# Kernel tuning notes

Hardware: AMD Instinct MI355X
Metric: run time of the kernel (lower is better)

Reference implementation:

```python
import jax, jax.numpy as jnp
import numpy as np

DIM = 1024
KEY = 128
UV = 1024  # dim * mlp_ratio // 2
SCALE = 1.0 / np.sqrt(KEY).astype(np.float32)
NEG_INF = 1e12


def _sinusoidal(n, d):
    # RoPE tables: sin/cos of shape [n, d//2]
    pos = np.arange(n)[:, None].astype(np.float32)
    inv = (1.0 / 10000 ** (np.arange(0, d, 2).astype(np.float32) / d))[None, :]
    ang = pos * inv
    return jnp.asarray(np.sin(ang)), jnp.asarray(np.cos(ang))


def setup_inputs() -> dict:
    key = jax.random.key(0)
    ks = jax.random.split(key, 4)
    B, N = 4, 2048
    hidden_states = jax.random.normal(ks[0], (B, N, DIM), dtype=jnp.float32)
    attention_mask = jax.random.randint(ks[1], (B, N, N), 0, 2).astype(jnp.int32)
    sin, cos = _sinusoidal(N, KEY)
    Wi = jax.random.normal(ks[2], (DIM, UV * 2 + KEY), dtype=jnp.float32) * (DIM ** -0.5)
    bi = jnp.zeros((UV * 2 + KEY,), jnp.float32)
    Wo = jax.random.normal(ks[3], (UV, DIM), dtype=jnp.float32) * (UV ** -0.5)
    bo = jnp.zeros((DIM,), jnp.float32)
    return {
        "hidden_states": hidden_states, "attention_mask": attention_mask,
        "sin": sin, "cos": cos, "Wi": Wi, "bi": bi, "Wo": Wo, "bo": bo,
        "q_gamma": jnp.ones((KEY,), jnp.float32), "q_beta": jnp.zeros((KEY,), jnp.float32),
        "k_gamma": jnp.ones((KEY,), jnp.float32), "k_beta": jnp.zeros((KEY,), jnp.float32),
    }


def _rotary(x, sin, cos):
    # x: [b, n, d]; sin/cos: [n, d//2]; interleaved RoPE, concat layout
    x1, x2 = x[..., 0::2], x[..., 1::2]
    return jnp.concatenate([x1 * cos - x2 * sin, x1 * sin + x2 * cos], axis=-1)


def reference(hidden_states, attention_mask, sin, cos, Wi, bi, Wo, bo,
              q_gamma, q_beta, k_gamma, k_beta):
    x = jax.nn.silu(hidden_states @ Wi + bi)            # [b, n, 2176]
    u, v, qk = x[..., :UV], x[..., UV:2 * UV], x[..., 2 * UV:]
    q = _rotary(qk * q_gamma + q_beta, sin, cos)        # [b, n, 128]
    k = _rotary(qk * k_gamma + k_beta, sin, cos)
    a = jnp.einsum('bmd,bnd->bmn', q, k) * SCALE        # [b, m, n]
    mask = attention_mask != 0
    a = jnp.where(mask, a, -NEG_INF)
    ll = attention_mask.sum(-1, keepdims=True).astype(a.dtype)  # [b, m, 1]
    A = jnp.square(jax.nn.relu(a)) / ll                 # squared_relu normalize
    out = (u * jnp.einsum('bmn,bnd->bmd', A, v)) @ Wo + bo
    return out
```

## Files before the change

kernel.cpp:

```cpp
#include <hip/hip_runtime.h>
#include <hip/hip_bf16.h>
#include <cstdint>

#define DIM   1024
#define KEY   128
#define UV    1024
#define NCOL  (UV*2 + KEY)
#define SEQ   2048
#define BATCH 4
#define MTOT  (BATCH*SEQ)
#define SCALE 0.08838834764831845f

typedef __attribute__((ext_vector_type(8))) short short8;
typedef __attribute__((ext_vector_type(4))) float f32x4;

__device__ inline unsigned short f2b(float x) {
  unsigned int u = __float_as_uint(x);
  unsigned int r = (u + 0x7fffu + ((u >> 16) & 1u)) >> 16;
  return (unsigned short)r;
}
__device__ inline float b2f(unsigned short x) {
  return __uint_as_float(((unsigned int)x) << 16);
}

__device__ inline void gload_lds16(const void* g, void* l) {
  __builtin_amdgcn_global_load_lds(
      (const __attribute__((address_space(1))) unsigned int*)g,
      (__attribute__((address_space(3))) unsigned int*)l, 16, 0, 0);
}

__device__ __forceinline__ void gemm128(
    const unsigned short* __restrict__ A, int lda,
    const unsigned short* __restrict__ Bt, int ldb,
    int K, f32x4 acc[4][4], unsigned short* lds) {
  const int tid  = threadIdx.x;
  const int lane = tid & 63;
  const int wid  = tid >> 6;
  const int wr   = wid >> 1, wc = wid & 1;
  const int fr   = lane & 15;
  const int fq   = lane >> 4;

#pragma unroll
  for (int i = 0; i < 4; ++i)
#pragma unroll
    for (int j = 0; j < 4; ++j) acc[i][j] = (f32x4){0.f, 0.f, 0.f, 0.f};

  auto stage = [&](int k, int d) {
    unsigned short* la = lds + d * 8192;
    unsigned short* lb = la + 4096;
#pragma unroll
    for (int p = 0; p < 2; ++p) {
      int c = p * 256 + tid;
      int r = c >> 2, q = c & 3;
      int qs = q ^ ((r >> 1) & 3);
      gload_lds16(A + (size_t)r * lda + k * 32 + qs * 8,
                  la + (size_t)(p * 256 + wid * 64) * 8);
    }
#pragma unroll
    for (int p = 0; p < 2; ++p) {
      int c = p * 256 + tid;
      int r = c >> 2, q = c & 3;
      int qs = q ^ ((r >> 1) & 3);
      gload_lds16(Bt + (size_t)r * ldb + k * 32 + qs * 8,
                  lb + (size_t)(p * 256 + wid * 64) * 8);
    }
  };

  const int slot = (fq ^ ((fr >> 1) & 3)) * 8;
  const int rA   = (wr * 64 + fr) * 32 + slot;
  const int rB   = (wc * 64 + fr) * 32 + slot;

  const int NK = K >> 5;
  stage(0, 0);
  for (int k = 0; k < NK; ++k) {
    const int d = k & 1;
    if (k + 1 < NK) {
      stage(k + 1, d ^ 1);
      asm volatile("s_waitcnt vmcnt(4)" ::: "memory");
    } else {
      asm volatile("s_waitcnt vmcnt(0)" ::: "memory");
    }
    __builtin_amdgcn_s_barrier();
    asm volatile("" ::: "memory");
    const unsigned short* la = lds + d * 8192;
    const unsigned short* lb = la + 4096;
    short8 af[4], bf[4];
#pragma unroll
    for (int s = 0; s < 4; ++s) {
      af[s] = *(const short8*)&la[rA + s * 512];
      bf[s] = *(const short8*)&lb[rB + s * 512];
    }
#pragma unroll
    for (int i = 0; i < 4; ++i)
#pragma unroll
      for (int j = 0; j < 4; ++j)
        acc[i][j] = __builtin_amdgcn_mfma_f32_16x16x32_bf16(af[i], bf[j], acc[i][j], 0, 0, 0);
    asm volatile("" ::: "memory");
    __builtin_amdgcn_s_barrier();
    asm volatile("" ::: "memory");
  }
}

#define EPILOGUE_COORDS()                      \
  const int lane = threadIdx.x & 63;           \
  const int wid  = threadIdx.x >> 6;           \
  const int wr   = wid >> 1, wc = wid & 1;     \
  const int fr   = lane & 15;                  \
  const int fq   = lane >> 4;

__device__ __forceinline__ void xcd_swz(int& tx, int& ty) {
  const int gx = gridDim.x, gy = gridDim.y;
  const int n = gx * gy;
  const int D = blockIdx.y * gx + blockIdx.x;
  const int c = (D & 7) * (n >> 3) + (D >> 3);
  tx = c / gy;
  ty = c - tx * gy;
}

#define PREP_CVT   8192
#define PREP_MASK  2048
#define PREP_TWI   2176
#define PREP_TWO   1024

__global__ __launch_bounds__(256) void k_prep(
    const float* __restrict__ h, unsigned short* __restrict__ hbf,
    const int* __restrict__ mask, float* __restrict__ ll, unsigned int* __restrict__ mb,
    const float* __restrict__ Wi, unsigned short* __restrict__ WiT,
    const float* __restrict__ Wo, unsigned short* __restrict__ WoT) {
  __shared__ float t[32][33];
  const int bid = blockIdx.x;
  const int tid = threadIdx.x;

  if (bid < PREP_CVT) {
    int id = bid * 256 + tid;
    float4 f = ((const float4*)h)[id];
    ushort4 o;
    o.x = f2b(f.x); o.y = f2b(f.y); o.z = f2b(f.z); o.w = f2b(f.w);
    ((ushort4*)hbf)[id] = o;
  } else if (bid < PREP_CVT + PREP_MASK) {
    int wid = tid >> 6, lane = tid & 63;
    int row = (bid - PREP_CVT) * 4 + wid;
    const int4* p = (const int4*)(mask + (size_t)row * SEQ);
    int s = 0;
#pragma unroll
    for (int i = 0; i < 8; ++i) {
      int4 v = p[i * 64 + lane];
      unsigned nib = (v.x != 0 ? 1u : 0u) | (v.y != 0 ? 2u : 0u) |
                     (v.z != 0 ? 4u : 0u) | (v.w != 0 ? 8u : 0u);
      unsigned w = 0;
#pragma unroll
      for (int k2 = 0; k2 < 8; ++k2)
        w |= __shfl(nib, (lane & ~7) + k2, 64) << (4 * k2);
      if ((lane & 7) == 0) mb[(size_t)row * 64 + i * 8 + (lane >> 3)] = w;
      s += v.x + v.y + v.z + v.w;
    }
    for (int off = 32; off; off >>= 1) s += __shfl_down(s, off);
    if (lane == 0) ll[row] = (float)s;
  } else {
    const float* in; unsigned short* outp; int R, C, bx, by;
    if (bid < PREP_CVT + PREP_MASK + PREP_TWI) {
      int b = bid - (PREP_CVT + PREP_MASK);
      in = Wi; outp = WiT; R = DIM; C = NCOL; bx = b % 68; by = b / 68;
    } else {
      int b = bid - (PREP_CVT + PREP_MASK + PREP_TWI);
      in = Wo; outp = WoT; R = DIM; C = UV; bx = b & 31; by = b >> 5;
    }
    int c0 = bx * 32, r0 = by * 32;
    int tx = tid & 31, ty = tid >> 5;
#pragma unroll
    for (int i = 0; i < 4; ++i)
      t[ty + i * 8][tx] = in[(size_t)(r0 + ty + i * 8) * C + c0 + tx];
    __syncthreads();
#pragma unroll
    for (int i = 0; i < 4; ++i)
      outp[(size_t)(c0 + ty + i * 8) * R + r0 + tx] = f2b(t[tx][ty + i * 8]);
  }
}

__global__ __launch_bounds__(256) void k_vT(const unsigned short* __restrict__ v,
                                            unsigned short* __restrict__ vT) {
  __shared__ unsigned short t[64][65];
  int b = blockIdx.z;
  int n0 = blockIdx.x * 64;
  int d0 = blockIdx.y * 64;
  int tid = threadIdx.x;
  int r = tid >> 4;
  int c4 = (tid & 15) * 4;
#pragma unroll
  for (int i = 0; i < 4; ++i) {
    int n = n0 + r + i * 16;
    ushort4 val = *(const ushort4*)&v[((size_t)b * SEQ + n) * UV + d0 + c4];
    t[c4 + 0][r + i * 16] = val.x;
    t[c4 + 1][r + i * 16] = val.y;
    t[c4 + 2][r + i * 16] = val.z;
    t[c4 + 3][r + i * 16] = val.w;
  }
  __syncthreads();
#pragma unroll
  for (int i = 0; i < 4; ++i) {
    int d = d0 + r + i * 16;
    ushort4 o;
    o.x = t[r + i * 16][c4 + 0];
    o.y = t[r + i * 16][c4 + 1];
    o.z = t[r + i * 16][c4 + 2];
    o.w = t[r + i * 16][c4 + 3];
    *(ushort4*)&vT[((size_t)b * UV + d) * SEQ + n0 + c4] = o;
  }
}

__global__ __launch_bounds__(256, 4) void k_gemm1(const unsigned short* __restrict__ hbf,
                                                  const unsigned short* __restrict__ WiT,
                                                  const float* __restrict__ bi,
                                                  const float* __restrict__ sn,
                                                  const float* __restrict__ cs,
                                                  const float* __restrict__ qg,
                                                  const float* __restrict__ qb,
                                                  const float* __restrict__ kg,
                                                  const float* __restrict__ kb,
                                                  unsigned short* __restrict__ u,
                                                  unsigned short* __restrict__ v,
                                                  unsigned short* __restrict__ qbuf,
                                                  unsigned short* __restrict__ kbuf) {
  __shared__ unsigned short lds[16384];
  int tx, ty; xcd_swz(tx, ty);
  int m0 = tx * 128, n0 = ty * 128;
  f32x4 acc[4][4];
  gemm128(hbf + (size_t)m0 * DIM, DIM, WiT + (size_t)n0 * DIM, DIM, DIM, acc, lds);
  EPILOGUE_COORDS();
  if (n0 < 2 * UV) {
#pragma unroll
    for (int i = 0; i < 4; ++i)
#pragma unroll
      for (int j = 0; j < 4; ++j)
#pragma unroll
        for (int r = 0; r < 4; ++r) {
          int row = m0 + wr * 64 + i * 16 + fq * 4 + r;
          int col = n0 + wc * 64 + j * 16 + fr;
          float x = acc[i][j][r] + bi[col];
          float s = x / (1.f + __expf(-x));
          if (n0 < UV) u[(size_t)row * UV + col] = f2b(s);
          else         v[(size_t)row * UV + col - UV] = f2b(s);
        }
  } else {
    const int colk_base = wc * 64;
    const bool ev = (fr & 1) == 0;
#pragma unroll
    for (int i = 0; i < 4; ++i)
#pragma unroll
      for (int j = 0; j < 4; ++j)
#pragma unroll
        for (int r = 0; r < 4; ++r) {
          int row  = m0 + wr * 64 + i * 16 + fq * 4 + r;
          int colk = colk_base + j * 16 + fr;
          float x = acc[i][j][r] + bi[2 * UV + colk];
          float s = x / (1.f + __expf(-x));
          float aq = s * qg[colk] + qb[colk];
          float ak = s * kg[colk] + kb[colk];
          float aqx = __shfl_xor(aq, 1);
          float akx = __shfl_xor(ak, 1);
          int t_ = colk >> 1;
          int n  = row & (SEQ - 1);
          float cc = cs[n * 64 + t_], ss = sn[n * 64 + t_];
          float q1 = ev ? aq : aqx, q2 = ev ? aqx : aq;
          float k1 = ev ? ak : akx, k2 = ev ? akx : ak;
          float resq = ev ? (q1 * cc - q2 * ss) : (q1 * ss + q2 * cc);
          float resk = ev ? (k1 * cc - k2 * ss) : (k1 * ss + k2 * cc);
          int oc = ev ? t_ : (64 + t_);
          qbuf[(size_t)row * KEY + oc] = f2b(resq);
          kbuf[(size_t)row * KEY + oc] = f2b(resk);
        }
  }
}

__global__ __launch_bounds__(256, 4) void k_qk(const unsigned short* __restrict__ q,
                                               const unsigned short* __restrict__ k,
                                               const unsigned int* __restrict__ mb,
                                               const float* __restrict__ ll,
                                               unsigned short* __restrict__ Abuf) {
  __shared__ unsigned short lds[16384];
  int b = blockIdx.z;
  int tx, ty; xcd_swz(tx, ty);
  int m0 = tx * 128, n0 = ty * 128;
  f32x4 acc[4][4];
  gemm128(q + ((size_t)b * SEQ + m0) * KEY, KEY,
          k + ((size_t)b * SEQ + n0) * KEY, KEY, KEY, acc, lds);
  EPILOGUE_COORDS();
#pragma unroll
  for (int i = 0; i < 4; ++i)
#pragma unroll
    for (int r = 0; r < 4; ++r) {
      int row = m0 + wr * 64 + i * 16 + fq * 4 + r;
      size_t rb = (size_t)b * SEQ + row;
      unsigned long long mw =
          *(const unsigned long long*)&mb[rb * 64 + (n0 >> 5) + wc * 2];
      float rll = 1.0f / ll[rb];
#pragma unroll
      for (int j = 0; j < 4; ++j) {
        int col = n0 + wc * 64 + j * 16 + fr;
        float a = acc[i][j][r] * SCALE;
        bool on = (mw >> (j * 16 + fr)) & 1ull;
        float rel = (on && a > 0.f) ? a : 0.f;
        Abuf[rb * SEQ + col] = f2b(rel * rel * rll);
      }
    }
}

__global__ __launch_bounds__(256, 4) void k_av(const unsigned short* __restrict__ Abuf,
                                               const unsigned short* __restrict__ vT,
                                               const unsigned short* __restrict__ u,
                                               unsigned short* __restrict__ g) {
  __shared__ unsigned short lds[16384];
  int b = blockIdx.z;
  int tx, ty; xcd_swz(tx, ty);
  int m0 = tx * 128, n0 = ty * 128;
  f32x4 acc[4][4];
  gemm128(Abuf + ((size_t)b * SEQ + m0) * SEQ, SEQ,
          vT + ((size_t)b * UV + n0) * SEQ, SEQ, SEQ, acc, lds);
  EPILOGUE_COORDS();
#pragma unroll
  for (int i = 0; i < 4; ++i)
#pragma unroll
    for (int j = 0; j < 4; ++j)
#pragma unroll
      for (int r = 0; r < 4; ++r) {
        int row = m0 + wr * 64 + i * 16 + fq * 4 + r;
        int col = n0 + wc * 64 + j * 16 + fr;
        size_t gi = ((size_t)b * SEQ + row) * UV + col;
        g[gi] = f2b(acc[i][j][r] * b2f(u[gi]));
      }
}

__global__ __launch_bounds__(256, 4) void k_out(const unsigned short* __restrict__ g,
                                                const unsigned short* __restrict__ WoT,
                                                const float* __restrict__ bo,
                                                float* __restrict__ out) {
  __shared__ unsigned short lds[16384];
  int tx, ty; xcd_swz(tx, ty);
  int m0 = tx * 128, n0 = ty * 128;
  f32x4 acc[4][4];
  gemm128(g + (size_t)m0 * UV, UV, WoT + (size_t)n0 * UV, UV, UV, acc, lds);
  EPILOGUE_COORDS();
#pragma unroll
  for (int i = 0; i < 4; ++i)
#pragma unroll
    for (int j = 0; j < 4; ++j)
#pragma unroll
      for (int r = 0; r < 4; ++r) {
        int row = m0 + wr * 64 + i * 16 + fq * 4 + r;
        int col = n0 + wc * 64 + j * 16 + fr;
        out[(size_t)row * DIM + col] = acc[i][j][r] + bo[col];
      }
}

extern "C" void kernel_launch(void* const* d_in, const int* in_sizes, int n_in,
                              void* d_out, int out_size, void* d_ws, size_t ws_size,
                              hipStream_t stream) {
  const float* h    = (const float*)d_in[0];
  const int*   mask = (const int*)d_in[1];
  const float* sn   = (const float*)d_in[2];
  const float* cs   = (const float*)d_in[3];
  const float* Wi   = (const float*)d_in[4];
  const float* bi   = (const float*)d_in[5];
  const float* Wo   = (const float*)d_in[6];
  const float* bo   = (const float*)d_in[7];
  const float* qg   = (const float*)d_in[8];
  const float* qb   = (const float*)d_in[9];
  const float* kg   = (const float*)d_in[10];
  const float* kb   = (const float*)d_in[11];
  float* out = (float*)d_out;

  char* ws = (char*)d_ws;
  size_t off = 0;
  auto alloc = [&](size_t bytes) { void* p = ws + off; off += (bytes + 255) & ~(size_t)255; return p; };
  unsigned short* hbf  = (unsigned short*)alloc((size_t)MTOT * DIM * 2);
  unsigned short* WiT  = (unsigned short*)alloc((size_t)NCOL * DIM * 2);
  unsigned short* WoT  = (unsigned short*)alloc((size_t)DIM * UV * 2);
  unsigned short* u    = (unsigned short*)alloc((size_t)MTOT * UV * 2);
  unsigned short* v    = (unsigned short*)alloc((size_t)MTOT * UV * 2);
  unsigned short* vT   = (unsigned short*)alloc((size_t)MTOT * UV * 2);
  unsigned short* qbuf = (unsigned short*)alloc((size_t)MTOT * KEY * 2);
  unsigned short* kbuf = (unsigned short*)alloc((size_t)MTOT * KEY * 2);
  float*          ll   = (float*)alloc((size_t)MTOT * 4);
  unsigned int*   mbits= (unsigned int*)alloc((size_t)MTOT * 64 * 4);
  unsigned short* Abuf = (unsigned short*)alloc((size_t)BATCH * SEQ * SEQ * 2);
  unsigned short* g    = (unsigned short*)alloc((size_t)MTOT * UV * 2);

  k_prep<<<PREP_CVT + PREP_MASK + PREP_TWI + PREP_TWO, 256, 0, stream>>>(
      h, hbf, mask, ll, mbits, Wi, WiT, Wo, WoT);

  k_gemm1<<<dim3(MTOT / 128, NCOL / 128), 256, 0, stream>>>(
      hbf, WiT, bi, sn, cs, qg, qb, kg, kb, u, v, qbuf, kbuf);
  k_vT<<<dim3(SEQ / 64, UV / 64, BATCH), 256, 0, stream>>>(v, vT);
  k_qk<<<dim3(SEQ / 128, SEQ / 128, BATCH), 256, 0, stream>>>(qbuf, kbuf, mbits, ll, Abuf);
  k_av<<<dim3(SEQ / 128, UV / 128, BATCH), 256, 0, stream>>>(Abuf, vT, u, g);
  k_out<<<dim3(MTOT / 128, DIM / 128), 256, 0, stream>>>(g, WoT, bo, out);
}
```

Before: 182.6 us.

## Fuse v transpose into gemm1 epilogue via LDS staging

Blocks of gemm1 that produce the v columns now stage the SiLU outputs transposed in shared memory and write vT directly, using 16-byte row stores. This removes the separate k_vT kernel, its launch, and one full round trip of the v tensor through global memory. The LDS allocation grows slightly to hold the 128x136 padded tile. The staging buffer reuses LDS right after gemm128, which is safe only if gemm128 ends with a barrier.

```diff
diff --git a/kernel.cpp b/kernel.cpp
--- a/kernel.cpp
+++ b/kernel.cpp
@@ -177,37 +177,6 @@
   }
 }
 
-__global__ __launch_bounds__(256) void k_vT(const unsigned short* __restrict__ v,
-                                            unsigned short* __restrict__ vT) {
-  __shared__ unsigned short t[64][65];
-  int b = blockIdx.z;
-  int n0 = blockIdx.x * 64;
-  int d0 = blockIdx.y * 64;
-  int tid = threadIdx.x;
-  int r = tid >> 4;
-  int c4 = (tid & 15) * 4;
-#pragma unroll
-  for (int i = 0; i < 4; ++i) {
-    int n = n0 + r + i * 16;
-    ushort4 val = *(const ushort4*)&v[((size_t)b * SEQ + n) * UV + d0 + c4];
-    t[c4 + 0][r + i * 16] = val.x;
-    t[c4 + 1][r + i * 16] = val.y;
-    t[c4 + 2][r + i * 16] = val.z;
-    t[c4 + 3][r + i * 16] = val.w;
-  }
-  __syncthreads();
-#pragma unroll
-  for (int i = 0; i < 4; ++i) {
-    int d = d0 + r + i * 16;
-    ushort4 o;
-    o.x = t[r + i * 16][c4 + 0];
-    o.y = t[r + i * 16][c4 + 1];
-    o.z = t[r + i * 16][c4 + 2];
-    o.w = t[r + i * 16][c4 + 3];
-    *(ushort4*)&vT[((size_t)b * UV + d) * SEQ + n0 + c4] = o;
-  }
-}
-
 __global__ __launch_bounds__(256, 4) void k_gemm1(const unsigned short* __restrict__ hbf,
                                                   const unsigned short* __restrict__ WiT,
                                                   const float* __restrict__ bi,
@@ -218,16 +187,16 @@
                                                   const float* __restrict__ kg,
                                                   const float* __restrict__ kb,
                                                   unsigned short* __restrict__ u,
-                                                  unsigned short* __restrict__ v,
+                                                  unsigned short* __restrict__ vT,
                                                   unsigned short* __restrict__ qbuf,
                                                   unsigned short* __restrict__ kbuf) {
-  __shared__ unsigned short lds[16384];
+  __shared__ unsigned short lds[17408];
   int tx, ty; xcd_swz(tx, ty);
   int m0 = tx * 128, n0 = ty * 128;
   f32x4 acc[4][4];
   gemm128(hbf + (size_t)m0 * DIM, DIM, WiT + (size_t)n0 * DIM, DIM, DIM, acc, lds);
   EPILOGUE_COORDS();
-  if (n0 < 2 * UV) {
+  if (n0 < UV) {
 #pragma unroll
     for (int i = 0; i < 4; ++i)
 #pragma unroll
@@ -238,9 +207,38 @@
           int col = n0 + wc * 64 + j * 16 + fr;
           float x = acc[i][j][r] + bi[col];
           float s = x / (1.f + __expf(-x));
-          if (n0 < UV) u[(size_t)row * UV + col] = f2b(s);
-          else         v[(size_t)row * UV + col - UV] = f2b(s);
+          u[(size_t)row * UV + col] = f2b(s);
         }
+  } else if (n0 < 2 * UV) {
+    unsigned short (*t)[136] = (unsigned short (*)[136])lds;
+#pragma unroll
+    for (int i = 0; i < 4; ++i)
+#pragma unroll
+      for (int j = 0; j < 4; ++j)
+#pragma unroll
+        for (int r = 0; r < 4; r += 2) {
+          int rl = wr * 64 + i * 16 + fq * 4 + r;
+          int dl = wc * 64 + j * 16 + fr;
+          int col = n0 + dl;
+          float x0 = acc[i][j][r]     + bi[col];
+          float x1 = acc[i][j][r + 1] + bi[col];
+          float s0 = x0 / (1.f + __expf(-x0));
+          float s1 = x1 / (1.f + __expf(-x1));
+          unsigned pk = (unsigned)f2b(s0) | ((unsigned)f2b(s1) << 16);
+          *(unsigned*)&t[dl][rl] = pk;
+        }
+    __syncthreads();
+    int bb = m0 >> 11;
+    int ns = m0 & (SEQ - 1);
+    int d0 = n0 - UV;
+    const int tid = threadIdx.x;
+#pragma unroll
+    for (int it = 0; it < 8; ++it) {
+      int idx = it * 256 + tid;
+      int dl = idx >> 4, q = idx & 15;
+      *(int4*)&vT[((size_t)bb * UV + d0 + dl) * SEQ + ns + q * 8] =
+          *(const int4*)&t[dl][q * 8];
+    }
   } else {
     const int colk_base = wc * 64;
     const bool ev = (fr & 1) == 0;
@@ -376,7 +374,6 @@
   unsigned short* WiT  = (unsigned short*)alloc((size_t)NCOL * DIM * 2);
   unsigned short* WoT  = (unsigned short*)alloc((size_t)DIM * UV * 2);
   unsigned short* u    = (unsigned short*)alloc((size_t)MTOT * UV * 2);
-  unsigned short* v    = (unsigned short*)alloc((size_t)MTOT * UV * 2);
   unsigned short* vT   = (unsigned short*)alloc((size_t)MTOT * UV * 2);
   unsigned short* qbuf = (unsigned short*)alloc((size_t)MTOT * KEY * 2);
   unsigned short* kbuf = (unsigned short*)alloc((size_t)MTOT * KEY * 2);
@@ -389,8 +386,7 @@
       h, hbf, mask, ll, mbits, Wi, WiT, Wo, WoT);
 
   k_gemm1<<<dim3(MTOT / 128, NCOL / 128), 256, 0, stream>>>(
-      hbf, WiT, bi, sn, cs, qg, qb, kg, kb, u, v, qbuf, kbuf);
-  k_vT<<<dim3(SEQ / 64, UV / 64, BATCH), 256, 0, stream>>>(v, vT);
+      hbf, WiT, bi, sn, cs, qg, qb, kg, kb, u, vT, qbuf, kbuf);
   k_qk<<<dim3(SEQ / 128, SEQ / 128, BATCH), 256, 0, stream>>>(qbuf, kbuf, mbits, ll, Abuf);
   k_av<<<dim3(SEQ / 128, UV / 128, BATCH), 256, 0, stream>>>(Abuf, vT, u, g);
   k_out<<<dim3(MTOT / 128, DIM / 128), 256, 0, stream>>>(g, WoT, bo, out);
```

Result: no change. 180.3 us (-1.3%).
